# Performance work log

Measured on AMD Instinct MI355X. Metric: run time of the kernel, lower is better.

## Reference

```python
import jax, jax.numpy as jnp
import numpy as np

R = 32
BN_EPS = 1e-5


def _bn(x, g, b):
    # eval-mode BatchNorm with running_mean=0, running_var=1
    shp = (1, -1) + (1,) * (x.ndim - 2)
    scale = g / np.float32(np.sqrt(1.0 + BN_EPS))
    return x * scale.reshape(shp) + b.reshape(shp)


def _conv3d(x, w, b):
    y = jax.lax.conv_general_dilated(x, w, (1, 1, 1), [(1, 1)] * 3,
                                     dimension_numbers=('NCDHW', 'OIDHW', 'NCDHW'))
    return y + b[None, :, None, None, None]


def _conv1d(x, w, b):  # kernel_size=1 conv -> matmul; w [O,I], x [B,I,N]
    return jnp.einsum('oi,bin->bon', w, x) + b[None, :, None]


def _voxelize(features, coords, r):
    # PVCNN Voxelization: detach coords, center, normalize, scatter-average
    coords = jax.lax.stop_gradient(coords)
    c = coords - coords.mean(axis=2, keepdims=True)            # [B,3,N]
    nrm = jnp.linalg.norm(c, axis=1, keepdims=True)            # [B,1,N]
    c = c / (nrm.max(axis=2, keepdims=True) * 2.0) + 0.5
    c = jnp.clip(c * r, 0.0, r - 1.0)                          # float voxel coords
    vox = jnp.round(c).astype(jnp.int32)
    B, C, N = features.shape
    idx = vox[:, 0] * r * r + vox[:, 1] * r + vox[:, 2]        # [B,N]
    flat = (idx + (jnp.arange(B, dtype=jnp.int32) * (r ** 3))[:, None]).reshape(-1)
    feats = features.transpose(0, 2, 1).reshape(B * N, C)
    sums = jax.ops.segment_sum(feats, flat, num_segments=B * r ** 3)
    cnt = jax.ops.segment_sum(jnp.ones((B * N,), features.dtype), flat, num_segments=B * r ** 3)
    grid = sums / jnp.maximum(cnt, 1.0)[:, None]
    grid = grid.reshape(B, r, r, r, C).transpose(0, 4, 1, 2, 3)  # [B,C,r,r,r]
    return grid, c


def _devoxelize(grid, c, r):
    # trilinear interpolation gather at float coords c in [0, r-1]
    B, C = grid.shape[:2]
    lo = jnp.clip(jnp.floor(c).astype(jnp.int32), 0, r - 1)
    hi = jnp.minimum(lo + 1, r - 1)
    f = c - lo.astype(c.dtype)
    gridf = grid.reshape(B, C, r * r * r)
    gather = jax.vmap(lambda g, i: g[:, i])  # per-batch [C,R3],[N] -> [C,N]
    out = jnp.zeros((B, C, c.shape[2]), grid.dtype)
    for ix, wx in ((lo[:, 0], 1.0 - f[:, 0]), (hi[:, 0], f[:, 0])):
        for iy, wy in ((lo[:, 1], 1.0 - f[:, 1]), (hi[:, 1], f[:, 1])):
            for iz, wz in ((lo[:, 2], 1.0 - f[:, 2]), (hi[:, 2], f[:, 2])):
                idx = ix * r * r + iy * r + iz
                out = out + gather(gridf, idx) * (wx * wy * wz)[:, None, :]
    return out


def setup_inputs() -> dict:
    key = jax.random.key(0)
    ks = jax.random.split(key, 24)
    n = lambda k, s, sc=0.05: (jax.random.normal(k, s, dtype=jnp.float32) * sc)
    inp = {
        'features': jax.random.normal(ks[0], (4, 64, 65536), dtype=jnp.float32),
        'coords': jax.random.normal(ks[1], (4, 3, 65536), dtype=jnp.float32),
        'vconv_w': n(ks[2], (64, 64, 3, 3, 3)),
        'vconv_b': n(ks[3], (64,)),
        'vbn_g': 1.0 + n(ks[4], (64,)),
        'vbn_b': n(ks[5], (64,)),
        'res_w': n(ks[6], (2, 2, 64, 64, 3, 3, 3)),
        'res_b': n(ks[7], (2, 2, 64)),
        'res_bn_g': 1.0 + n(ks[8], (2, 2, 64)),
        'res_bn_b': n(ks[9], (2, 2, 64)),
        'pf_w': n(ks[10], (64, 64)),
        'pf_b': n(ks[11], (64,)),
        'pf_bn_g': 1.0 + n(ks[12], (64,)),
        'pf_bn_b': n(ks[13], (64,)),
        'attn_wa': n(ks[14], (16, 64)),
        'attn_ba': n(ks[15], (16,)),
        'attn_wb': n(ks[16], (16, 64)),
        'attn_bb': n(ks[17], (16,)),
        'attn_wc': n(ks[18], (1, 32)),
        'attn_bc': n(ks[19], (1,)),
    }
    return inp


def reference(features, coords, vconv_w, vconv_b, vbn_g, vbn_b,
              res_w, res_b, res_bn_g, res_bn_b,
              pf_w, pf_b, pf_bn_g, pf_bn_b,
              attn_wa, attn_ba, attn_wb, attn_bb, attn_wc, attn_bc):
    grid, nc = _voxelize(features, coords, R)
    # BasicConvolutionBlock
    x = jax.nn.relu(_bn(_conv3d(grid, vconv_w, vconv_b), vbn_g, vbn_b))
    # two ResidualBlocks (inc==outc, stride 1 -> identity downsample)
    for i in range(2):
        y = jax.nn.relu(_bn(_conv3d(x, res_w[i, 0], res_b[i, 0]), res_bn_g[i, 0], res_bn_b[i, 0]))
        y = _bn(_conv3d(y, res_w[i, 1], res_b[i, 1]), res_bn_g[i, 1], res_bn_b[i, 1])
        x = jax.nn.relu(y + x)
    vfeat = _devoxelize(x, nc, R)                               # [B,64,N]
    # SharedMLP: Conv1d(k=1) + BN1d + ReLU
    pfeat = jax.nn.relu(_bn(_conv1d(features, pf_w, pf_b), pf_bn_g, pf_bn_b))
    # Attn fusion (channel dim 64 -> atten_64 branch)
    xa = _conv1d(vfeat, attn_wa, attn_ba)
    xb = _conv1d(pfeat, attn_wb, attn_bb)
    q = _conv1d(jnp.concatenate([xa, xb], axis=1), attn_wc, attn_bc)
    attention = 1.0 + jax.nn.sigmoid(q)
    fused = vfeat * attention + pfeat
    return fused
```

## Files before the change

kernel.cpp:

```cpp
#include <hip/hip_runtime.h>
#include <math.h>

#define NPT 65536
#define NB 4
#define R3 32768

typedef __attribute__((ext_vector_type(8))) short short8;
typedef __attribute__((ext_vector_type(16))) float f32x16;

#define OFF_WB16 0
#define OFF_BEFF 276480
#define OFF_PWB  276800
#define OFF_PB   280896
#define OFF_WAE  280960
#define OFF_WBE  281024
#define OFF_Q0   281088
#define OFF_MEAN 281104
#define OFF_MAXN 281116
#define OFF_PART 281120
#define OFF_AUX  281248
#define OFF_CB3  281504
#define OFF_CUR  1067936
#define OFF_ORD  1199008
#define OFF_GA   1330080
#define OFF_G0   9718688
#define OFF_G1   13912992

__device__ __forceinline__ unsigned short f2b(float f) {
    union { float f; unsigned int u; } v; v.f = f;
    unsigned int r = v.u + 0x7fffu + ((v.u >> 16) & 1u);
    return (unsigned short)(r >> 16);
}
__device__ __forceinline__ float b2f(unsigned short u) {
    union { unsigned int u; float f; } v; v.u = ((unsigned int)u) << 16; return v.f;
}

__global__ void k_setup(const float* __restrict__ vconv_w, const float* __restrict__ vconv_b,
                        const float* __restrict__ vbn_g, const float* __restrict__ vbn_b,
                        const float* __restrict__ res_w, const float* __restrict__ res_b,
                        const float* __restrict__ res_bn_g, const float* __restrict__ res_bn_b,
                        const float* __restrict__ pf_w, const float* __restrict__ pf_b,
                        const float* __restrict__ pf_bn_g, const float* __restrict__ pf_bn_b,
                        const float* __restrict__ wa, const float* __restrict__ ba,
                        const float* __restrict__ wb, const float* __restrict__ bb,
                        const float* __restrict__ wc, const float* __restrict__ bc,
                        float* __restrict__ ws) {
    int idx = blockIdx.x * 256 + threadIdx.x;
    const float invs = rsqrtf(1.00001f);
    if (idx < 552960) {
        unsigned short* wb16 = (unsigned short*)(ws + OFF_WB16);
        int j = idx & 7;
        int l = (idx >> 3) & 63;
        int nh = (idx >> 9) & 1;
        int ks = (idx >> 10) & 3;
        int rest = idx >> 12;
        int t = rest % 27;
        int layer = rest / 27;
        int i = ks * 16 + ((l >> 5) << 3) + j;
        int o = nh * 32 + (l & 31);
        float scale, wsrc;
        if (layer == 0) {
            scale = vbn_g[o] * invs;
            wsrc = vconv_w[(o * 64 + i) * 27 + t];
        } else {
            scale = res_bn_g[(layer - 1) * 64 + o] * invs;
            wsrc = res_w[(size_t)(layer - 1) * 110592 + (o * 64 + i) * 27 + t];
        }
        wb16[idx] = f2b(wsrc * scale);
        return;
    }
    idx -= 552960;
    if (idx < 320) {
        int l = idx >> 6, o = idx & 63;
        float b_, g_, s_;
        if (l == 0) { b_ = vconv_b[o]; g_ = vbn_g[o]; s_ = vbn_b[o]; }
        else {
            b_ = res_b[(l - 1) * 64 + o];
            g_ = res_bn_g[(l - 1) * 64 + o];
            s_ = res_bn_b[(l - 1) * 64 + o];
        }
        ws[OFF_BEFF + idx] = b_ * g_ * invs + s_;
    } else if (idx < 4416) {
        int e = idx - 320;
        int j = e & 7;
        int lane = (e >> 3) & 63;
        int ks = (e >> 9) & 3;
        int half = e >> 11;
        int i = ks * 16 + ((lane >> 5) << 3) + j;
        int o = half * 32 + (lane & 31);
        ((unsigned short*)(ws + OFF_PWB))[e] = f2b(pf_w[o * 64 + i] * pf_bn_g[o] * invs);
    } else if (idx < 4480) {
        int o = idx - 4416;
        ws[OFF_PB + o] = pf_b[o] * pf_bn_g[o] * invs + pf_bn_b[o];
    } else if (idx < 4544) {
        int o = idx - 4480;
        float s = 0.f;
        for (int j = 0; j < 16; j++) s += wc[j] * wa[j * 64 + o];
        ws[OFF_WAE + o] = s;
    } else if (idx < 4608) {
        int o = idx - 4544;
        float s = 0.f;
        for (int j = 0; j < 16; j++) s += wc[16 + j] * wb[j * 64 + o];
        ws[OFF_WBE + o] = s;
    } else if (idx == 4608) {
        float s = bc[0];
        for (int j = 0; j < 16; j++) s += wc[j] * ba[j] + wc[16 + j] * bb[j];
        ws[OFF_Q0] = s;
    }
}

__global__ __launch_bounds__(256) void k_mean1(const float* __restrict__ coords,
                                               float* __restrict__ part,
                                               float4* __restrict__ curz) {
    for (int i = blockIdx.x * 256 + threadIdx.x; i < 32768; i += 96 * 256)
        curz[i] = make_float4(0.f, 0.f, 0.f, 0.f);
    __shared__ float sm[256];
    int bd = blockIdx.x >> 3, chunk = blockIdx.x & 7;
    int tid = threadIdx.x;
    const float* p = coords + (size_t)bd * NPT + chunk * 8192;
    float s = 0.f;
    for (int n = tid; n < 8192; n += 256) s += p[n];
    sm[tid] = s; __syncthreads();
    for (int st = 128; st > 0; st >>= 1) {
        if (tid < st) sm[tid] += sm[tid + st];
        __syncthreads();
    }
    if (tid == 0) part[blockIdx.x] = sm[0];
}

__global__ __launch_bounds__(256) void k_maxn1(const float* __restrict__ coords,
                                               float* __restrict__ part,
                                               float* __restrict__ mean) {
    __shared__ float sm[256];
    int b = blockIdx.x >> 3, chunk = blockIdx.x & 7;
    int tid = threadIdx.x;
    float m0 = 0.f, m1 = 0.f, m2 = 0.f;
    #pragma unroll
    for (int c = 0; c < 8; c++) {
        m0 += part[(b * 3 + 0) * 8 + c];
        m1 += part[(b * 3 + 1) * 8 + c];
        m2 += part[(b * 3 + 2) * 8 + c];
    }
    m0 *= (1.0f / NPT); m1 *= (1.0f / NPT); m2 *= (1.0f / NPT);
    if (chunk == 0 && tid == 0) {
        mean[b * 3] = m0; mean[b * 3 + 1] = m1; mean[b * 3 + 2] = m2;
    }
    const float* p0 = coords + (size_t)(b * 3) * NPT + chunk * 8192;
    float mx = 0.f;
    for (int n = tid; n < 8192; n += 256) {
        float dx = p0[n] - m0, dy = p0[NPT + n] - m1, dz = p0[2 * NPT + n] - m2;
        mx = fmaxf(mx, dx * dx + dy * dy + dz * dz);
    }
    sm[tid] = mx; __syncthreads();
    for (int st = 128; st > 0; st >>= 1) {
        if (tid < st) sm[tid] = fmaxf(sm[tid], sm[tid + st]);
        __syncthreads();
    }
    if (tid == 0) part[96 + blockIdx.x] = sm[0];
}

__global__ void k_prep(const float* __restrict__ coords, const float* __restrict__ mean,
                       const float* __restrict__ part, float* __restrict__ cb3,
                       int* __restrict__ cursor) {
    int gid = blockIdx.x * 256 + threadIdx.x;
    int b = gid >> 16, n = gid & 65535;
    float mx = 0.f;
    #pragma unroll
    for (int c = 0; c < 8; c++) mx = fmaxf(mx, part[96 + b * 8 + c]);
    float inv = 0.5f / sqrtf(mx);
    float c0 = (coords[(size_t)(b * 3) * NPT + n]     - mean[b * 3])     * inv + 0.5f;
    float c1 = (coords[(size_t)(b * 3 + 1) * NPT + n] - mean[b * 3 + 1]) * inv + 0.5f;
    float c2 = (coords[(size_t)(b * 3 + 2) * NPT + n] - mean[b * 3 + 2]) * inv + 0.5f;
    c0 = fminf(fmaxf(c0 * 32.f, 0.f), 31.f);
    c1 = fminf(fmaxf(c1 * 32.f, 0.f), 31.f);
    c2 = fminf(fmaxf(c2 * 32.f, 0.f), 31.f);
    cb3[gid * 3]     = c0;
    cb3[gid * 3 + 1] = c1;
    cb3[gid * 3 + 2] = c2;
    int vx = b * R3 + ((int)rintf(c0) * 1024 + (int)rintf(c1) * 32 + (int)rintf(c2));
    atomicAdd(&cursor[vx], 1);
}

__global__ void k_scan1(int* __restrict__ cur, int* __restrict__ aux) {
    __shared__ int sm[256];
    int t = threadIdx.x;
    int base = blockIdx.x * 512 + t * 2;
    int c0 = cur[base], c1 = cur[base + 1];
    int s = c0 + c1;
    sm[t] = s; __syncthreads();
    for (int off = 1; off < 256; off <<= 1) {
        int v = (t >= off) ? sm[t - off] : 0;
        __syncthreads();
        sm[t] += v;
        __syncthreads();
    }
    int ex = sm[t] - s;
    cur[base] = ex;
    cur[base + 1] = ex + c0;
    if (t == 255) aux[blockIdx.x] = sm[t];
}

__global__ void k_scan3(int* __restrict__ cur, const int* __restrict__ aux) {
    __shared__ int sm[256];
    int t = threadIdx.x;
    sm[t] = (t < blockIdx.x) ? aux[t] : 0;
    __syncthreads();
    for (int off = 128; off > 0; off >>= 1) {
        if (t < off) sm[t] += sm[t + off];
        __syncthreads();
    }
    int add = sm[0];
    int base = blockIdx.x * 512 + t * 2;
    cur[base] += add;
    cur[base + 1] += add;
}

__global__ __launch_bounds__(256) void k_trans(const float* __restrict__ feats,
                                               unsigned short* __restrict__ ft) {
    __shared__ float lds[64][65];
    int b = blockIdx.x >> 10;
    int n0 = (blockIdx.x & 1023) << 6;
    int tid = threadIdx.x;
    int nl = tid & 63;
    #pragma unroll
    for (int it = 0; it < 16; it++) {
        int ch = it * 4 + (tid >> 6);
        lds[nl][ch] = feats[((size_t)(b * 64 + ch) << 16) + n0 + nl];
    }
    __syncthreads();
    int nn = tid >> 2;
    int ch0 = (tid & 3) << 4;
    size_t obase = (((size_t)(b << 16) + n0 + nn) << 6) + ch0;
    short8 v0, v1;
    #pragma unroll
    for (int j = 0; j < 8; j++) v0[j] = (short)f2b(lds[nn][ch0 + j]);
    #pragma unroll
    for (int j = 0; j < 8; j++) v1[j] = (short)f2b(lds[nn][ch0 + 8 + j]);
    *(short8*)(ft + obase) = v0;
    *(short8*)(ft + obase + 8) = v1;
}

__global__ void k_place(const float* __restrict__ cb3, int* __restrict__ cursor,
                        unsigned short* __restrict__ order) {
    int gid = blockIdx.x * 256 + threadIdx.x;
    int b = gid >> 16;
    float c0 = cb3[gid * 3], c1 = cb3[gid * 3 + 1], c2 = cb3[gid * 3 + 2];
    int vx = b * R3 + ((int)rintf(c0) * 1024 + (int)rintf(c1) * 32 + (int)rintf(c2));
    int slot = atomicAdd(&cursor[vx], 1);
    order[slot] = (unsigned short)(gid & 65535);
}

__global__ __launch_bounds__(256) void k_gather(const int* __restrict__ cursor,
        const unsigned short* __restrict__ order, const unsigned short* __restrict__ ft,
        unsigned short* __restrict__ g0) {
    int tid = threadIdx.x;
    int lane = tid & 63;
    int v = lane >> 5;
    int p = (lane >> 3) & 3;
    int g = lane & 7;
    int vx = (blockIdx.x * 4 + (tid >> 6)) * 2 + v;
    int e = cursor[vx];
    int s = (vx == 0) ? 0 : cursor[vx - 1];
    int cnt = e - s;
    int bb = vx >> 15;
    float acc[8] = {0.f, 0.f, 0.f, 0.f, 0.f, 0.f, 0.f, 0.f};
    for (int base = s; base < e; base += 4) {
        int idx = base + p;
        if (idx < e) {
            int n = order[idx];
            const unsigned short* fp = ft + (((size_t)(bb << 16) + n) << 6) + (g << 3);
            short8 vv = *(const short8*)fp;
            #pragma unroll
            for (int j = 0; j < 8; j++) acc[j] += b2f((unsigned short)vv[j]);
        }
    }
    #pragma unroll
    for (int j = 0; j < 8; j++) {
        acc[j] += __shfl_xor(acc[j], 8, 64);
        acc[j] += __shfl_xor(acc[j], 16, 64);
    }
    if (p == 0) {
        float inv = 1.0f / (float)max(cnt, 1);
        int col = vx >> 5, z = vx & 31;
        short8 o8;
        #pragma unroll
        for (int j = 0; j < 8; j++) o8[j] = (short)f2b(acc[j] * inv);
        *(short8*)(g0 + (size_t)col * 2048 + (g << 8) + z * 8) = o8;
    }
}

__global__ __launch_bounds__(512, 2) void k_conv(const unsigned short* __restrict__ in,
        const unsigned short* __restrict__ w, const float* __restrict__ bias,
        const float* __restrict__ idF, float* __restrict__ outF,
        unsigned short* __restrict__ out, int zmaj) {
    __shared__ unsigned short sA[18 * 2048 + 32];
    int tid = threadIdx.x;
    int lane = tid & 63;
    int wid = tid >> 6;
    int cp = wid & 1;
    int nh = (wid >> 1) & 1;
    int kh = wid >> 2;
    int tile = blockIdx.x;
    int b = blockIdx.y;
    int x = tile >> 3;
    int y0 = (tile & 7) << 2;
    int t = tid & 255;
    int h = tid >> 8;
    int sq = wid & 3;

    if (tid < 4) ((float*)sA)[18432 + tid] = 0.f;

    const unsigned short* wl = w + nh * 512 + kh * 2048 + lane * 8;
    short8 wbuf[4];
    #pragma unroll
    for (int s = 0; s < 3; s++)
        wbuf[s] = *(const short8*)(wl + (s / 6) * 12288 + ((s % 6) / 2) * 4096 + (s & 1) * 1024);

    #pragma unroll 1
    for (int s2 = 0; s2 < 9; s2++) {
        int s = s2 * 2 + h;
        int gx = x + s / 6 - 1;
        int gy = y0 + s % 6 - 1;
        if ((unsigned)gx < 32u && (unsigned)gy < 32u) {
            const unsigned short* gsrc = in + (((size_t)b * 1024 + gx * 32 + gy) << 11)
                                            + ((size_t)t << 3);
            __builtin_amdgcn_global_load_lds(
                (const __attribute__((address_space(1))) unsigned int*)gsrc,
                (__attribute__((address_space(3))) unsigned int*)(sA + s * 2048 + (sq << 9)),
                16, 0, 0);
        } else {
            ((float4*)(sA + s * 2048))[t] = make_float4(0.f, 0.f, 0.f, 0.f);
        }
    }
    __syncthreads();

    f32x16 accA = {}, accB = {};
    int half = lane >> 5;
    int z = lane & 31;
    int abase = (half << 8) + kh * 1024;
    short8 a0buf[2], a1buf[2];
    {
        int zz = z - 1;
        bool zv = zz >= 0;
        int base = (cp * 2) * 2048 + abase;
        int a0 = zv ? (base + zz * 8) : 36864;
        int a1 = zv ? (base + 2048 + zz * 8) : 36864;
        a0buf[0] = *(const short8*)(sA + a0);
        a1buf[0] = *(const short8*)(sA + a1);
    }
    #pragma unroll
    for (int s = 0; s < 54; s++) {
        if (s < 53) {
            int sn = s + 1;
            int c9 = sn / 6, dzi = (sn % 6) / 2;
            int zz = z + dzi - 1;
            bool zv = (unsigned)zz < 32u;
            int s0 = (c9 / 3) * 6 + (c9 % 3) + cp * 2;
            int base = s0 * 2048 + abase + (sn & 1) * 512;
            int a0 = zv ? (base + zz * 8) : 36864;
            int a1 = zv ? (base + 2048 + zz * 8) : 36864;
            a0buf[sn & 1] = *(const short8*)(sA + a0);
            a1buf[sn & 1] = *(const short8*)(sA + a1);
        }
        if (s < 51) {
            int sw = s + 3;
            wbuf[sw & 3] = *(const short8*)(wl + (sw / 6) * 12288
                                             + ((sw % 6) / 2) * 4096 + (sw & 1) * 1024);
        }
        __builtin_amdgcn_sched_barrier(0);
        accA = __builtin_amdgcn_mfma_f32_32x32x16_bf16(a0buf[s & 1], wbuf[s & 3], accA, 0, 0, 0);
        accB = __builtin_amdgcn_mfma_f32_32x32x16_bf16(a1buf[s & 1], wbuf[s & 3], accB, 0, 0, 0);
    }

    __syncthreads();
    float* RED = (float*)sA;
    int o = nh * 32 + (lane & 31);
    #pragma unroll
    for (int cc = 0; cc < 2; cc++) {
        const f32x16& acc = cc ? accB : accA;
        int col = cp * 2 + cc;
        #pragma unroll
        for (int r = 0; r < 16; r++) {
            int zr = (r & 3) + ((r >> 2) << 3) + ((lane >> 5) << 2);
            RED[((kh * 4 + col) * 32 + zr) * 65 + o] = acc[r];
        }
    }
    __syncthreads();
    #pragma unroll
    for (int e = 0; e < 2; e++) {
        int idx = e * 512 + tid;
        int col = idx >> 8;
        int g = (idx >> 5) & 7;
        int z2 = idx & 31;
        const float* r0 = RED + ((0 * 4 + col) * 32 + z2) * 65 + g * 8;
        const float* r1 = RED + ((1 * 4 + col) * 32 + z2) * 65 + g * 8;
        int outcol = b * 1024 + x * 32 + y0 + col;
        size_t cbase = (size_t)outcol << 11;
        size_t swz = cbase + g * 256 + z2 * 8;
        float vv[8];
        #pragma unroll
        for (int j = 0; j < 8; j++) vv[j] = r0[j] + r1[j] + bias[g * 8 + j];
        if (idF) {
            #pragma unroll
            for (int j = 0; j < 8; j++) vv[j] += idF[swz + j];
        }
        #pragma unroll
        for (int j = 0; j < 8; j++) vv[j] = fmaxf(vv[j], 0.f);
        short8 o8;
        #pragma unroll
        for (int j = 0; j < 8; j++) o8[j] = (short)f2b(vv[j]);
        if (zmaj) *(short8*)(out + cbase + z2 * 64 + g * 8) = o8;
        else      *(short8*)(out + swz) = o8;
        if (outF) {
            #pragma unroll
            for (int j = 0; j < 8; j++) outF[swz + j] = vv[j];
        }
    }
}

__global__ __launch_bounds__(256) void k_pfeat(const float* __restrict__ feats,
        const float* __restrict__ pb, const unsigned short* __restrict__ pwb,
        unsigned short* __restrict__ pf) {
    int tid = threadIdx.x;
    int lane = tid & 63;
    int wv = tid >> 6;
    int tile = blockIdx.x * 4 + wv;
    int b = tile >> 11;
    int n0 = (tile & 2047) << 5;
    int m = lane & 31, kg = lane >> 5;
    const float* fb = feats + ((size_t)b << 22) + n0 + m;
    f32x16 acc0 = {}, acc1 = {};
    #pragma unroll
    for (int ks = 0; ks < 4; ks++) {
        short8 af;
        #pragma unroll
        for (int j = 0; j < 8; j++)
            af[j] = (short)f2b(fb[(size_t)(ks * 16 + kg * 8 + j) << 16]);
        short8 b0 = *(const short8*)(pwb + ((size_t)(ks * 64 + lane) << 3));
        short8 b1 = *(const short8*)(pwb + ((size_t)((4 + ks) * 64 + lane) << 3));
        acc0 = __builtin_amdgcn_mfma_f32_32x32x16_bf16(af, b0, acc0, 0, 0, 0);
        acc1 = __builtin_amdgcn_mfma_f32_32x32x16_bf16(af, b1, acc1, 0, 0, 0);
    }
    int och = lane & 31;
    float bias0 = pb[och], bias1 = pb[32 + och];
    #pragma unroll
    for (int r = 0; r < 16; r++) {
        int p = (r & 3) + ((r >> 2) << 3) + ((lane >> 5) << 2);
        size_t base = ((size_t)(b << 16) + n0 + p) << 6;
        pf[base + och]      = f2b(fmaxf(acc0[r] + bias0, 0.f));
        pf[base + 32 + och] = f2b(fmaxf(acc1[r] + bias1, 0.f));
    }
}

__global__ __launch_bounds__(256) void k_final(const float* __restrict__ cb3,
        const unsigned short* __restrict__ gb, const unsigned short* __restrict__ pfeat,
        const float* __restrict__ ws, float* __restrict__ out) {
    int tid = threadIdx.x;
    int lane = tid & 63;
    int g = lane >> 3;
    int p = lane & 7;
    int b = blockIdx.y;
    int nb = (blockIdx.x << 6) + ((tid >> 6) << 4) + p;
    float vf[2][8], pfv[2][8], part[2];
    const float* wae = ws + OFF_WAE + (g << 3);
    const float* wbe = ws + OFF_WBE + (g << 3);
    #pragma unroll
    for (int q = 0; q < 2; q++) {
        int n = nb + q * 8;
        int gid = (b << 16) + n;
        float c0 = cb3[gid * 3], c1 = cb3[gid * 3 + 1], c2 = cb3[gid * 3 + 2];
        int lx = (int)floorf(c0), ly = (int)floorf(c1), lz = (int)floorf(c2);
        int hx = min(lx + 1, 31), hy = min(ly + 1, 31), hz = min(lz + 1, 31);
        float fx = c0 - (float)lx, fy = c1 - (float)ly, fz = c2 - (float)lz;
        int xs[2] = {lx, hx}; float wxx[2] = {1.f - fx, fx};
        int ys[2] = {ly, hy}; float wyy[2] = {1.f - fy, fy};
        int zs[2] = {lz, hz}; float wzz[2] = {1.f - fz, fz};
        #pragma unroll
        for (int j = 0; j < 8; j++) vf[q][j] = 0.f;
        #pragma unroll
        for (int ii = 0; ii < 2; ii++)
        #pragma unroll
        for (int jj = 0; jj < 2; jj++)
        #pragma unroll
        for (int kk = 0; kk < 2; kk++) {
            float wgt = wxx[ii] * wyy[jj] * wzz[kk];
            const unsigned short* gp = gb + (((size_t)b * 1024 + xs[ii] * 32 + ys[jj]) << 11)
                                          + zs[kk] * 64 + (g << 3);
            short8 v = *(const short8*)gp;
            #pragma unroll
            for (int j = 0; j < 8; j++) vf[q][j] += wgt * b2f((unsigned short)v[j]);
        }
        const unsigned short* pp = pfeat + ((size_t)gid << 6) + (g << 3);
        short8 pv = *(const short8*)pp;
        #pragma unroll
        for (int j = 0; j < 8; j++) pfv[q][j] = b2f((unsigned short)pv[j]);
        float pt = 0.f;
        #pragma unroll
        for (int j = 0; j < 8; j++) pt += wae[j] * vf[q][j] + wbe[j] * pfv[q][j];
        part[q] = pt;
    }
    #pragma unroll
    for (int q = 0; q < 2; q++) {
        part[q] += __shfl_xor(part[q], 8, 64);
        part[q] += __shfl_xor(part[q], 16, 64);
        part[q] += __shfl_xor(part[q], 32, 64);
    }
    float q0 = part[0] + ws[OFF_Q0];
    float q1 = part[1] + ws[OFF_Q0];
    float at0 = 1.0f + 1.0f / (1.0f + expf(-q0));
    float at1 = 1.0f + 1.0f / (1.0f + expf(-q1));
    float* op0 = out + (((size_t)(b * 64 + (g << 3))) << 16) + nb;
    float* op1 = op0 + 8;
    #pragma unroll
    for (int j = 0; j < 8; j++) {
        op0[(size_t)j << 16] = vf[0][j] * at0 + pfv[0][j];
        op1[(size_t)j << 16] = vf[1][j] * at1 + pfv[1][j];
    }
}

extern "C" void kernel_launch(void* const* d_in, const int* in_sizes, int n_in,
                              void* d_out, int out_size, void* d_ws, size_t ws_size,
                              hipStream_t stream) {
    const float* features = (const float*)d_in[0];
    const float* coords   = (const float*)d_in[1];
    const float* vconv_w  = (const float*)d_in[2];
    const float* vconv_b  = (const float*)d_in[3];
    const float* vbn_g    = (const float*)d_in[4];
    const float* vbn_b    = (const float*)d_in[5];
    const float* res_w    = (const float*)d_in[6];
    const float* res_b    = (const float*)d_in[7];
    const float* res_bn_g = (const float*)d_in[8];
    const float* res_bn_b = (const float*)d_in[9];
    const float* pf_w     = (const float*)d_in[10];
    const float* pf_b     = (const float*)d_in[11];
    const float* pf_bn_g  = (const float*)d_in[12];
    const float* pf_bn_b  = (const float*)d_in[13];
    const float* attn_wa  = (const float*)d_in[14];
    const float* attn_ba  = (const float*)d_in[15];
    const float* attn_wb  = (const float*)d_in[16];
    const float* attn_bb  = (const float*)d_in[17];
    const float* attn_wc  = (const float*)d_in[18];
    const float* attn_bc  = (const float*)d_in[19];
    float* ws  = (float*)d_ws;
    float* out = (float*)d_out;

    unsigned short* WB  = (unsigned short*)(ws + OFF_WB16);
    unsigned short* PWB = (unsigned short*)(ws + OFF_PWB);
    int*            CUR = (int*)(ws + OFF_CUR);
    int*            AUX = (int*)(ws + OFF_AUX);
    unsigned short* ORD = (unsigned short*)(ws + OFF_ORD);
    unsigned short* FT  = (unsigned short*)(ws + OFF_GA);
    unsigned short* PF  = (unsigned short*)(ws + OFF_GA);
    float* GA = ws + OFF_GA;
    unsigned short* G0 = (unsigned short*)(ws + OFF_G0);
    unsigned short* G1 = (unsigned short*)(ws + OFF_G1);
    const float* Bv = ws + OFF_BEFF;

    k_setup<<<2179, 256, 0, stream>>>(vconv_w, vconv_b, vbn_g, vbn_b, res_w, res_b,
                                      res_bn_g, res_bn_b, pf_w, pf_b, pf_bn_g, pf_bn_b,
                                      attn_wa, attn_ba, attn_wb, attn_bb, attn_wc, attn_bc, ws);
    k_mean1<<<96, 256, 0, stream>>>(coords, ws + OFF_PART, (float4*)CUR);
    k_maxn1<<<32, 256, 0, stream>>>(coords, ws + OFF_PART, ws + OFF_MEAN);
    k_prep<<<1024, 256, 0, stream>>>(coords, ws + OFF_MEAN, ws + OFF_PART,
                                     ws + OFF_CB3, CUR);
    k_scan1<<<256, 256, 0, stream>>>(CUR, AUX);
    k_scan3<<<256, 256, 0, stream>>>(CUR, AUX);
    k_trans<<<4096, 256, 0, stream>>>(features, FT);
    k_place<<<1024, 256, 0, stream>>>(ws + OFF_CB3, CUR, ORD);
    k_gather<<<16384, 256, 0, stream>>>(CUR, ORD, FT, G0);

    dim3 cg(256, 4);
    k_conv<<<cg, 512, 0, stream>>>(G0, WB + 0 * 110592, Bv + 0,   nullptr, GA,      G1, 0);
    k_conv<<<cg, 512, 0, stream>>>(G1, WB + 1 * 110592, Bv + 64,  nullptr, nullptr, G0, 0);
    k_conv<<<cg, 512, 0, stream>>>(G0, WB + 2 * 110592, Bv + 128, GA,      GA,      G1, 0);
    k_conv<<<cg, 512, 0, stream>>>(G1, WB + 3 * 110592, Bv + 192, nullptr, nullptr, G0, 0);
    k_conv<<<cg, 512, 0, stream>>>(G0, WB + 4 * 110592, Bv + 256, GA,      nullptr, G1, 1);

    k_pfeat<<<2048, 256, 0, stream>>>(features, ws + OFF_PB, PWB, PF);

    dim3 fg(1024, 4);
    k_final<<<fg, 256, 0, stream>>>(ws + OFF_CB3, G1, PF, ws, out);
}
```

Baseline: 504.6 us.

## Gather voxel averages per 128-voxel block using LDS atomics over point ranges

k_place now also records each point's local voxel id alongside the order array. k_gather is restructured from one half-wavefront per voxel into one block per 128 consecutive voxels. The block walks that contiguous range of sorted points with all four waves and accumulates into an LDS accumulator using shared-memory float atomics. This balances work across sparse and dense voxels and removes the many nearly empty wavefronts of the old grid. In exchange it adds LDS atomic contention and an extra voxid buffer that aliases G1.

```diff
diff --git a/kernel.cpp b/kernel.cpp
--- a/kernel.cpp
+++ b/kernel.cpp
@@ -241,51 +241,58 @@
 }
 
 __global__ void k_place(const float* __restrict__ cb3, int* __restrict__ cursor,
-                        unsigned short* __restrict__ order) {
+                        unsigned short* __restrict__ order,
+                        unsigned short* __restrict__ voxid) {
     int gid = blockIdx.x * 256 + threadIdx.x;
     int b = gid >> 16;
     float c0 = cb3[gid * 3], c1 = cb3[gid * 3 + 1], c2 = cb3[gid * 3 + 2];
-    int vx = b * R3 + ((int)rintf(c0) * 1024 + (int)rintf(c1) * 32 + (int)rintf(c2));
+    int lv = (int)rintf(c0) * 1024 + (int)rintf(c1) * 32 + (int)rintf(c2);
+    int vx = b * R3 + lv;
     int slot = atomicAdd(&cursor[vx], 1);
     order[slot] = (unsigned short)(gid & 65535);
+    voxid[slot] = (unsigned short)lv;
 }
 
 __global__ __launch_bounds__(256) void k_gather(const int* __restrict__ cursor,
-        const unsigned short* __restrict__ order, const unsigned short* __restrict__ ft,
-        unsigned short* __restrict__ g0) {
-    int tid = threadIdx.x;
+        const unsigned short* __restrict__ order, const unsigned short* __restrict__ voxid,
+        const unsigned short* __restrict__ ft, unsigned short* __restrict__ g0) {
+    __shared__ float acc[128][65];
+    int tid = threadIdx.x;
+    for (int i = tid; i < 128 * 65; i += 256) ((float*)acc)[i] = 0.f;
+    int vx0 = blockIdx.x << 7;
+    int bb = vx0 >> 15;
+    int lv0 = vx0 & 32767;
+    int s = (vx0 == 0) ? 0 : cursor[vx0 - 1];
+    int e = cursor[vx0 + 127];
+    __syncthreads();
     int lane = tid & 63;
-    int v = lane >> 5;
-    int p = (lane >> 3) & 3;
+    int p = lane >> 3;
     int g = lane & 7;
-    int vx = (blockIdx.x * 4 + (tid >> 6)) * 2 + v;
-    int e = cursor[vx];
-    int s = (vx == 0) ? 0 : cursor[vx - 1];
-    int cnt = e - s;
-    int bb = vx >> 15;
-    float acc[8] = {0.f, 0.f, 0.f, 0.f, 0.f, 0.f, 0.f, 0.f};
-    for (int base = s; base < e; base += 4) {
+    int wid = tid >> 6;
+    for (int base = s + wid * 8; base < e; base += 32) {
         int idx = base + p;
         if (idx < e) {
             int n = order[idx];
+            int lvx = (int)voxid[idx] - lv0;
             const unsigned short* fp = ft + (((size_t)(bb << 16) + n) << 6) + (g << 3);
-            short8 vv = *(const short8*)fp;
+            short8 v = *(const short8*)fp;
+            float* a = &acc[lvx][g << 3];
             #pragma unroll
-            for (int j = 0; j < 8; j++) acc[j] += b2f((unsigned short)vv[j]);
-        }
-    }
-    #pragma unroll
-    for (int j = 0; j < 8; j++) {
-        acc[j] += __shfl_xor(acc[j], 8, 64);
-        acc[j] += __shfl_xor(acc[j], 16, 64);
-    }
-    if (p == 0) {
+            for (int j = 0; j < 8; j++) atomicAdd(&a[j], b2f((unsigned short)v[j]));
+        }
+    }
+    __syncthreads();
+    for (int i = tid; i < 1024; i += 256) {
+        int lvx = i >> 3;
+        int gg = i & 7;
+        int vx = vx0 + lvx;
+        int cnt = cursor[vx] - ((vx == 0) ? 0 : cursor[vx - 1]);
         float inv = 1.0f / (float)max(cnt, 1);
+        short8 o8;
+        #pragma unroll
+        for (int j = 0; j < 8; j++) o8[j] = (short)f2b(acc[lvx][(gg << 3) + j] * inv);
         int col = vx >> 5, z = vx & 31;
-        short8 o8;
-        #pragma unroll
-        for (int j = 0; j < 8; j++) o8[j] = (short)f2b(acc[j] * inv);
-        *(short8*)(g0 + (size_t)col * 2048 + (g << 8) + z * 8) = o8;
+        *(short8*)(g0 + (size_t)col * 2048 + (gg << 8) + z * 8) = o8;
     }
 }
 
@@ -554,6 +561,7 @@
     float* GA = ws + OFF_GA;
     unsigned short* G0 = (unsigned short*)(ws + OFF_G0);
     unsigned short* G1 = (unsigned short*)(ws + OFF_G1);
+    unsigned short* VID = (unsigned short*)(ws + OFF_G1);
     const float* Bv = ws + OFF_BEFF;
 
     k_setup<<<2179, 256, 0, stream>>>(vconv_w, vconv_b, vbn_g, vbn_b, res_w, res_b,
@@ -566,8 +574,8 @@
     k_scan1<<<256, 256, 0, stream>>>(CUR, AUX);
     k_scan3<<<256, 256, 0, stream>>>(CUR, AUX);
     k_trans<<<4096, 256, 0, stream>>>(features, FT);
-    k_place<<<1024, 256, 0, stream>>>(ws + OFF_CB3, CUR, ORD);
-    k_gather<<<16384, 256, 0, stream>>>(CUR, ORD, FT, G0);
+    k_place<<<1024, 256, 0, stream>>>(ws + OFF_CB3, CUR, ORD, VID);
+    k_gather<<<1024, 256, 0, stream>>>(CUR, ORD, VID, FT, G0);
 
     dim3 cg(256, 4);
     k_conv<<<cg, 512, 0, stream>>>(G0, WB + 0 * 110592, Bv + 0,   nullptr, GA,      G1, 0);
```

After: 1.756 ms. 3.48x slower.
